# Performance work log

Hardware: AMD Instinct MI355X
Metric: run time of the kernel (lower is better)

## Reference

```python
import jax, jax.numpy as jnp
from jax import lax
import numpy as np

N_CLASS = 5
B, T = 2048, 2048


def setup_inputs() -> dict:
    key = jax.random.key(0)
    k1, k2 = jax.random.split(key)
    x = jax.random.normal(k1, (B, T, N_CLASS), dtype=jnp.float32)
    mask = jnp.ones((B, T), dtype=jnp.int32)
    transform = jax.random.normal(k2, (N_CLASS + 2, N_CLASS + 2), dtype=jnp.float32)
    return {"x": x, "mask": mask, "transform": transform}


def reference(x, mask, transform):
    # Batched Viterbi decode. x:[B,T,C], mask:[B,T], transform:[C+2,C+2]
    Bb, Tt, C = x.shape
    START, END = C, C + 1
    trans = transform[:C, :C]                      # [C,C] prev -> curr
    mb = mask.astype(bool)

    dp0 = x[:, 0, :] + transform[START, :C][None]  # [B,C]

    def step(dp, inp):
        xt, mt = inp                               # xt:[B,C], mt:[B]
        sc = dp[:, :, None] + trans[None]          # [B,C_prev,C_curr]
        bp = jnp.argmax(sc, axis=1)                # [B,C]
        new_dp = jnp.max(sc, axis=1) + xt          # [B,C]
        dp_out = jnp.where(mt[:, None], new_dp, dp)
        # identity backpointer on padded steps so backtrace is a no-op there
        bp_out = jnp.where(mt[:, None], bp, jnp.arange(C)[None, :])
        return dp_out, bp_out

    xs = (jnp.moveaxis(x[:, 1:, :], 1, 0),         # [T-1,B,C]
          jnp.moveaxis(mb[:, 1:], 1, 0))           # [T-1,B]
    dp, bps = lax.scan(step, dp0, xs)              # bps: [T-1,B,C]

    final = dp + transform[:C, END][None]          # [B,C]
    max_score = jnp.max(final, axis=1)             # [B]
    last = jnp.argmax(final, axis=1)               # [B]

    def back(idx, bp):
        prev = jnp.take_along_axis(bp, idx[:, None], axis=1)[:, 0]
        return prev, idx

    first, rest = lax.scan(back, last, bps, reverse=True)  # rest: [T-1,B]
    path = jnp.concatenate([first[None], rest], axis=0)    # [T,B]
    return max_score, path.T                                # [B], [B,T]
```

## Files before the change

### kernel.cpp

```cpp
#include <hip/hip_runtime.h>
#include <cstdint>

#define B_    2048
#define T_    2048
#define TD    7
#define NCHK  128
#define IDENT 0x4688u

__device__ __forceinline__ uint32_t mcompose(uint32_t f, uint32_t g) {
    uint32_t r = 0;
#pragma unroll
    for (int j = 0; j < 5; ++j) {
        uint32_t gj = (g >> (3 * j)) & 7u;
        r |= ((f >> (3 * gj)) & 7u) << (3 * j);
    }
    return r;
}

__device__ __forceinline__ uint32_t cvtpk(float lo, float hi) {
    uint32_t r;
    asm("v_cvt_pk_bf16_f32 %0, %1, %2" : "=v"(r) : "v"(lo), "v"(hi));
    return r;
}

__device__ __forceinline__ float bfld(const uint16_t* __restrict__ xs, int h) {
    return __uint_as_float(((uint32_t)xs[h]) << 16);
}

template<bool P>
__device__ __forceinline__ void hstep(const uint16_t* __restrict__ xs, int h, bool pred,
                                      float (&dp)[5], const float (&tr)[5][5]) {
    float nd[5];
#pragma unroll
    for (int j = 0; j < 5; ++j) {
        float v = fmaxf(fmaxf(fmaxf(fmaxf(dp[0] + tr[0][j], dp[1] + tr[1][j]),
                                    dp[2] + tr[2][j]), dp[3] + tr[3][j]),
                        dp[4] + tr[4][j]);
        nd[j] = v + bfld(xs, h + j);
    }
#pragma unroll
    for (int j = 0; j < 5; ++j) dp[j] = (P && !pred) ? dp[j] : nd[j];
}

template<bool SEL>
__device__ __forceinline__ uint32_t lstep(const uint16_t* __restrict__ xs, int h, bool mm,
                                          float (&dp)[5], const float (&tr)[5][5],
                                          uint32_t& rho) {
    float nd[5]; int aa[5]; uint32_t pk = 0;
#pragma unroll
    for (int j = 0; j < 5; ++j) {
        float s[5];
#pragma unroll
        for (int i = 0; i < 5; ++i) {
            float f = dp[i] + tr[i][j];
            uint32_t u = (__float_as_uint(f) & ~7u) | (uint32_t)(7 - i);
            s[i] = __uint_as_float(u);
        }
        float m = fmaxf(fmaxf(fmaxf(fmaxf(s[0], s[1]), s[2]), s[3]), s[4]);
        int a = 7 - (int)(__float_as_uint(m) & 7u);
        float v = m + bfld(xs, h + j);
        if (SEL) { a = mm ? a : j; nd[j] = mm ? v : dp[j]; }
        else     { nd[j] = v; }
        aa[j] = a;
        pk |= ((uint32_t)a) << (3 * j);
    }
    uint32_t nr = 0;
#pragma unroll
    for (int j = 0; j < 5; ++j) nr |= ((rho >> (3 * aa[j])) & 7u) << (3 * j);
    rho = nr;
#pragma unroll
    for (int j = 0; j < 5; ++j) dp[j] = nd[j];
    return pk;
}

template<bool AM>
__device__ __forceinline__ void fwd(const uint16_t* __restrict__ xs,
                                    const uint16_t* __restrict__ msk, int cc,
                                    const float (&tr)[5][5], const float (&ts)[5],
                                    float (&dp)[5], float (&dpE)[5],
                                    uint32_t (&acc)[8], uint32_t& rho) {
    const int hbase = (cc > 0) ? 82 * (cc - 1) : 0;
#pragma unroll
    for (int j = 0; j < 5; ++j) dp[j] = bfld(xs, hbase + j);
    if (cc <= 1) {
#pragma unroll
        for (int j = 0; j < 5; ++j) dp[j] += ts[j];
    }
    const uint32_t mh = AM ? 0xFFFFu : ((cc > 0) ? (uint32_t)msk[cc - 1] : 0u);
#pragma unroll
    for (int h = 1; h <= 15; ++h) {
        if (AM) hstep<false>(xs, hbase + 5 * h, true, dp, tr);
        else    hstep<true >(xs, hbase + 5 * h, ((mh >> h) & 1u) != 0, dp, tr);
    }
    if (AM && cc == 0) {
#pragma unroll
        for (int j = 0; j < 5; ++j) dp[j] = bfld(xs, j) + ts[j];
    }
#pragma unroll
    for (int j = 0; j < 5; ++j) dpE[j] = (cc == 0) ? 0.0f : dp[j];

    rho = IDENT;
    const int lb = 82 * cc;
    const uint32_t ml = AM ? 0xFFFFu : (uint32_t)msk[cc];
    acc[0] = lstep<true>(xs, lb, (cc != 0) && ((ml & 1u) != 0), dp, tr, rho);
#pragma unroll
    for (int l = 1; l < 16; ++l) {
        uint32_t pk;
        if (AM) pk = lstep<false>(xs, lb + 5 * l, true, dp, tr, rho);
        else    pk = lstep<true >(xs, lb + 5 * l, ((ml >> l) & 1u) != 0, dp, tr, rho);
        if (l & 1) acc[l >> 1] |= pk << 16;
        else       acc[l >> 1]  = pk;
    }
}

__global__ __launch_bounds__(128) void k_all(
    const float* __restrict__ x, const int* __restrict__ mask,
    const float* __restrict__ tf, float* __restrict__ out)
{
    __shared__ uint16_t xs[10496];
    __shared__ uint16_t msk[NCHK];
    __shared__ uint32_t tot[2];
    __shared__ float    part[2];
    __shared__ int      lastS;

    const int b = blockIdx.x, c = threadIdx.x;
    const int lane = c & 63, w = c >> 6;

    const float4* gx = (const float4*)(x + (size_t)b * (T_ * 5));
#pragma unroll
    for (int q = 0; q < 20; ++q) {
        int fi = c + 128 * q;
        float4 v = gx[fi];
        int e0 = 4 * fi;
        int k  = (e0 * 52429) >> 22;
        int h0 = e0 + 2 * k;
        *(uint32_t*)(xs + h0)     = cvtpk(v.x, v.y);
        *(uint32_t*)(xs + h0 + 2) = cvtpk(v.z, v.w);
    }
    uint32_t mb = 0;
    {
        const int4* gm = (const int4*)(mask + (size_t)b * T_);
#pragma unroll
        for (int q = 0; q < 4; ++q) {
            int4 a = gm[4 * c + q];
            mb |= (a.x ? 1u : 0u) << (4 * q);
            mb |= (a.y ? 1u : 0u) << (4 * q + 1);
            mb |= (a.z ? 1u : 0u) << (4 * q + 2);
            mb |= (a.w ? 1u : 0u) << (4 * q + 3);
        }
        msk[c] = (uint16_t)mb;
    }

    float tr[5][5], ts[5], te[5];
#pragma unroll
    for (int i = 0; i < 5; ++i)
#pragma unroll
        for (int j = 0; j < 5; ++j) tr[i][j] = tf[i * TD + j];
#pragma unroll
    for (int j = 0; j < 5; ++j) ts[j] = tf[5 * TD + j];
#pragma unroll
    for (int j = 0; j < 5; ++j) te[j] = tf[j * TD + 6];

    const int allones = __syncthreads_and(mb == 0xFFFFu);

    float dp[5], dpE[5]; uint32_t acc[8], rho;
    if (allones) fwd<true >(xs, msk, c, tr, ts, dp, dpE, acc, rho);
    else         fwd<false>(xs, msk, c, tr, ts, dp, dpE, acc, rho);

    float svec[5];
#pragma unroll
    for (int j = 0; j < 5; ++j) {
        int r = (rho >> (3 * j)) & 7;
        float e = dpE[0];
        e = (r == 1) ? dpE[1] : e;
        e = (r == 2) ? dpE[2] : e;
        e = (r == 3) ? dpE[3] : e;
        e = (r == 4) ? dpE[4] : e;
        svec[j] = dp[j] - e;
    }

    uint32_t I = rho;
#pragma unroll
    for (int d = 1; d < 64; d <<= 1) {
        uint32_t oth = __shfl_down(I, d);
        uint32_t cm  = mcompose(I, oth);
        I = (lane + d < 64) ? cm : I;
    }
    if (lane == 0) tot[w] = I;
    if (c == NCHK - 1) {
        float best = dp[0] + te[0]; int last = 0;
#pragma unroll
        for (int j = 1; j < 5; ++j) {
            float s = dp[j] + te[j];
            if (s > best) { best = s; last = j; }
        }
        lastS = last;
    }
    __syncthreads();

    uint32_t Tw = (w == 0) ? tot[1] : IDENT;
    uint32_t Ex = __shfl_down(I, 1);
    uint32_t M  = (lane < 63) ? mcompose(Ex, Tw) : Tw;
    const int last = lastS;
    const int ec = (M >> (3 * last)) & 7;

    {
        float v = svec[0];
        v = (ec == 1) ? svec[1] : v;
        v = (ec == 2) ? svec[2] : v;
        v = (ec == 3) ? svec[3] : v;
        v = (ec == 4) ? svec[4] : v;
        if (c == NCHK - 1) v += te[last];
#pragma unroll
        for (int off = 1; off < 64; off <<= 1) v += __shfl_xor(v, off);
        if (lane == 0) part[w] = v;
    }
    __syncthreads();
    if (c == 0) out[b] = part[0] + part[1];

    float pv[16];
    int e = ec;
#pragma unroll
    for (int l = 15; l >= 0; --l) {
        pv[l] = (float)e;
        uint32_t p = (acc[l >> 1] >> (16 * (l & 1))) & 0xFFFFu;
        e = (p >> (3 * e)) & 7;
    }
    float* path = out + B_ + (size_t)b * T_ + c * 16;
#pragma unroll
    for (int q = 0; q < 4; ++q) {
        float4 v; v.x = pv[4*q]; v.y = pv[4*q+1]; v.z = pv[4*q+2]; v.w = pv[4*q+3];
        ((float4*)path)[q] = v;
    }
}

extern "C" void kernel_launch(void* const* d_in, const int* in_sizes, int n_in,
                              void* d_out, int out_size, void* d_ws, size_t ws_size,
                              hipStream_t stream) {
    const float* x         = (const float*)d_in[0];
    const int*   mask      = (const int*)d_in[1];
    const float* transform = (const float*)d_in[2];
    float*       out       = (float*)d_out;

    hipLaunchKernelGGL(k_all, dim3(B_), dim3(128), 0, stream,
                       x, mask, transform, out);
}
```

Before: 40.68 us.

## Process two rows per block, prefetching the second row into registers during the first

Each block now handles two batch rows. The second row's x and mask are loaded into registers before the first row is computed, and a sched_barrier keeps those loads from sinking, so global-load latency overlaps the first row's forward pass. The shared buffer is refilled after a barrier. This halves the grid, sets launch bounds to a minimum of 2 blocks, and holds about 80 extra VGPRs for the prefetched data, which may lower occupancy.

```diff
diff --git a/kernel.cpp b/kernel.cpp
--- a/kernel.cpp
+++ b/kernel.cpp
@@ -26,6 +26,7 @@
 __device__ __forceinline__ float bfld(const uint16_t* __restrict__ xs, int h) {
     return __uint_as_float(((uint32_t)xs[h]) << 16);
 }
+
 
 template<bool P>
 __device__ __forceinline__ void hstep(const uint16_t* __restrict__ xs, int h, bool pred,
@@ -113,7 +114,125 @@
     }
 }
 
-__global__ __launch_bounds__(128) void k_all(
+template<bool AM>
+__device__ __forceinline__ void compute_row(
+    const uint16_t* __restrict__ xs, const uint16_t* __restrict__ msk,
+    uint32_t* __restrict__ tot, float* __restrict__ part, int* __restrict__ lastS,
+    int c, int lane, int w, int row,
+    const float (&tr)[5][5], const float (&ts)[5], const float (&te)[5],
+    float* __restrict__ out)
+{
+    float dp[5], dpE[5]; uint32_t acc[8], rho;
+    fwd<AM>(xs, msk, c, tr, ts, dp, dpE, acc, rho);
+
+    float svec[5];
+#pragma unroll
+    for (int j = 0; j < 5; ++j) {
+        int r = (rho >> (3 * j)) & 7;
+        float e = dpE[0];
+        e = (r == 1) ? dpE[1] : e;
+        e = (r == 2) ? dpE[2] : e;
+        e = (r == 3) ? dpE[3] : e;
+        e = (r == 4) ? dpE[4] : e;
+        svec[j] = dp[j] - e;
+    }
+
+    uint32_t I = rho;
+#pragma unroll
+    for (int d = 1; d < 64; d <<= 1) {
+        uint32_t oth = __shfl_down(I, d);
+        uint32_t cm  = mcompose(I, oth);
+        I = (lane + d < 64) ? cm : I;
+    }
+    if (lane == 0) tot[w] = I;
+    if (c == NCHK - 1) {
+        float best = dp[0] + te[0]; int last = 0;
+#pragma unroll
+        for (int j = 1; j < 5; ++j) {
+            float s = dp[j] + te[j];
+            if (s > best) { best = s; last = j; }
+        }
+        *lastS = last;
+    }
+    __syncthreads();
+
+    uint32_t Tw = (w == 0) ? tot[1] : IDENT;
+    uint32_t Ex = __shfl_down(I, 1);
+    uint32_t M  = (lane < 63) ? mcompose(Ex, Tw) : Tw;
+    const int last = *lastS;
+    const int ec = (M >> (3 * last)) & 7;
+
+    {
+        float v = svec[0];
+        v = (ec == 1) ? svec[1] : v;
+        v = (ec == 2) ? svec[2] : v;
+        v = (ec == 3) ? svec[3] : v;
+        v = (ec == 4) ? svec[4] : v;
+        if (c == NCHK - 1) v += te[last];
+#pragma unroll
+        for (int off = 1; off < 64; off <<= 1) v += __shfl_xor(v, off);
+        if (lane == 0) part[w] = v;
+    }
+    __syncthreads();
+    if (c == 0) out[row] = part[0] + part[1];
+
+    float pv[16];
+    int e = ec;
+#pragma unroll
+    for (int l = 15; l >= 0; --l) {
+        pv[l] = (float)e;
+        uint32_t p = (acc[l >> 1] >> (16 * (l & 1))) & 0xFFFFu;
+        e = (p >> (3 * e)) & 7;
+    }
+    float* path = out + B_ + (size_t)row * T_ + c * 16;
+#pragma unroll
+    for (int q = 0; q < 4; ++q) {
+        float4 v; v.x = pv[4*q]; v.y = pv[4*q+1]; v.z = pv[4*q+2]; v.w = pv[4*q+3];
+        ((float4*)path)[q] = v;
+    }
+}
+
+
+struct XR { float4 v[10]; };
+struct MR { int4 m[4]; };
+
+__device__ __forceinline__ void load_row(const float4* __restrict__ gx,
+                                         const int4* __restrict__ gm, int c,
+                                         XR& a, XR& b, MR& mr) {
+#pragma unroll
+    for (int q = 0; q < 10; ++q) a.v[q] = gx[c + 128 * q];
+#pragma unroll
+    for (int q = 0; q < 10; ++q) b.v[q] = gx[c + 128 * (10 + q)];
+#pragma unroll
+    for (int q = 0; q < 4; ++q) mr.m[q] = gm[4 * c + q];
+}
+
+__device__ __forceinline__ void write_half(uint16_t* __restrict__ xs, int c, int off,
+                                           const XR& r) {
+#pragma unroll
+    for (int q = 0; q < 10; ++q) {
+        int fi = c + 128 * (off + q);
+        int e0 = 4 * fi;
+        int k  = (e0 * 52429) >> 22;
+        int h0 = e0 + 2 * k;
+        *(uint32_t*)(xs + h0)     = cvtpk(r.v[q].x, r.v[q].y);
+        *(uint32_t*)(xs + h0 + 2) = cvtpk(r.v[q].z, r.v[q].w);
+    }
+}
+
+__device__ __forceinline__ uint32_t mask_bits(const MR& mr) {
+    uint32_t mb = 0;
+#pragma unroll
+    for (int q = 0; q < 4; ++q) {
+        mb |= (mr.m[q].x ? 1u : 0u) << (4 * q);
+        mb |= (mr.m[q].y ? 1u : 0u) << (4 * q + 1);
+        mb |= (mr.m[q].z ? 1u : 0u) << (4 * q + 2);
+        mb |= (mr.m[q].w ? 1u : 0u) << (4 * q + 3);
+    }
+    return mb;
+}
+
+__global__ __launch_bounds__(128, 2) void k_all(
     const float* __restrict__ x, const int* __restrict__ mask,
     const float* __restrict__ tf, float* __restrict__ out)
 {
@@ -123,33 +242,14 @@
     __shared__ float    part[2];
     __shared__ int      lastS;
 
-    const int b = blockIdx.x, c = threadIdx.x;
+    const int c = threadIdx.x;
     const int lane = c & 63, w = c >> 6;
-
-    const float4* gx = (const float4*)(x + (size_t)b * (T_ * 5));
-#pragma unroll
-    for (int q = 0; q < 20; ++q) {
-        int fi = c + 128 * q;
-        float4 v = gx[fi];
-        int e0 = 4 * fi;
-        int k  = (e0 * 52429) >> 22;
-        int h0 = e0 + 2 * k;
-        *(uint32_t*)(xs + h0)     = cvtpk(v.x, v.y);
-        *(uint32_t*)(xs + h0 + 2) = cvtpk(v.z, v.w);
-    }
-    uint32_t mb = 0;
-    {
-        const int4* gm = (const int4*)(mask + (size_t)b * T_);
-#pragma unroll
-        for (int q = 0; q < 4; ++q) {
-            int4 a = gm[4 * c + q];
-            mb |= (a.x ? 1u : 0u) << (4 * q);
-            mb |= (a.y ? 1u : 0u) << (4 * q + 1);
-            mb |= (a.z ? 1u : 0u) << (4 * q + 2);
-            mb |= (a.w ? 1u : 0u) << (4 * q + 3);
-        }
-        msk[c] = (uint16_t)mb;
-    }
+    const int row0 = 2 * blockIdx.x, row1 = row0 + 1;
+
+    const float4* gx0 = (const float4*)(x + (size_t)row0 * (T_ * 5));
+    const int4*   gm0 = (const int4*)(mask + (size_t)row0 * T_);
+    const float4* gx1 = (const float4*)(x + (size_t)row1 * (T_ * 5));
+    const int4*   gm1 = (const int4*)(mask + (size_t)row1 * T_);
 
     float tr[5][5], ts[5], te[5];
 #pragma unroll
@@ -161,77 +261,31 @@
 #pragma unroll
     for (int j = 0; j < 5; ++j) te[j] = tf[j * TD + 6];
 
-    const int allones = __syncthreads_and(mb == 0xFFFFu);
-
-    float dp[5], dpE[5]; uint32_t acc[8], rho;
-    if (allones) fwd<true >(xs, msk, c, tr, ts, dp, dpE, acc, rho);
-    else         fwd<false>(xs, msk, c, tr, ts, dp, dpE, acc, rho);
-
-    float svec[5];
-#pragma unroll
-    for (int j = 0; j < 5; ++j) {
-        int r = (rho >> (3 * j)) & 7;
-        float e = dpE[0];
-        e = (r == 1) ? dpE[1] : e;
-        e = (r == 2) ? dpE[2] : e;
-        e = (r == 3) ? dpE[3] : e;
-        e = (r == 4) ? dpE[4] : e;
-        svec[j] = dp[j] - e;
-    }
-
-    uint32_t I = rho;
-#pragma unroll
-    for (int d = 1; d < 64; d <<= 1) {
-        uint32_t oth = __shfl_down(I, d);
-        uint32_t cm  = mcompose(I, oth);
-        I = (lane + d < 64) ? cm : I;
-    }
-    if (lane == 0) tot[w] = I;
-    if (c == NCHK - 1) {
-        float best = dp[0] + te[0]; int last = 0;
-#pragma unroll
-        for (int j = 1; j < 5; ++j) {
-            float s = dp[j] + te[j];
-            if (s > best) { best = s; last = j; }
-        }
-        lastS = last;
-    }
+    XR a0, b0; MR mr0;
+    load_row(gx0, gm0, c, a0, b0, mr0);
+    write_half(xs, c, 0, a0);
+    write_half(xs, c, 10, b0);
+    uint32_t mb0 = mask_bits(mr0);
+    msk[c] = (uint16_t)mb0;
+    const int am0 = __syncthreads_and(mb0 == 0xFFFFu);
+
+    XR a1, b1; MR mr1;
+    load_row(gx1, gm1, c, a1, b1, mr1);
+    __builtin_amdgcn_sched_barrier(0);
+
+    if (am0) compute_row<true >(xs, msk, tot, part, &lastS, c, lane, w, row0, tr, ts, te, out);
+    else     compute_row<false>(xs, msk, tot, part, &lastS, c, lane, w, row0, tr, ts, te, out);
+
     __syncthreads();
 
-    uint32_t Tw = (w == 0) ? tot[1] : IDENT;
-    uint32_t Ex = __shfl_down(I, 1);
-    uint32_t M  = (lane < 63) ? mcompose(Ex, Tw) : Tw;
-    const int last = lastS;
-    const int ec = (M >> (3 * last)) & 7;
-
-    {
-        float v = svec[0];
-        v = (ec == 1) ? svec[1] : v;
-        v = (ec == 2) ? svec[2] : v;
-        v = (ec == 3) ? svec[3] : v;
-        v = (ec == 4) ? svec[4] : v;
-        if (c == NCHK - 1) v += te[last];
-#pragma unroll
-        for (int off = 1; off < 64; off <<= 1) v += __shfl_xor(v, off);
-        if (lane == 0) part[w] = v;
-    }
-    __syncthreads();
-    if (c == 0) out[b] = part[0] + part[1];
-
-    float pv[16];
-    int e = ec;
-#pragma unroll
-    for (int l = 15; l >= 0; --l) {
-        pv[l] = (float)e;
-        uint32_t p = (acc[l >> 1] >> (16 * (l & 1))) & 0xFFFFu;
-        e = (p >> (3 * e)) & 7;
-    }
-    float* path = out + B_ + (size_t)b * T_ + c * 16;
-#pragma unroll
-    for (int q = 0; q < 4; ++q) {
-        float4 v; v.x = pv[4*q]; v.y = pv[4*q+1]; v.z = pv[4*q+2]; v.w = pv[4*q+3];
-        ((float4*)path)[q] = v;
-    }
+    write_half(xs, c, 0, a1);
+    write_half(xs, c, 10, b1);
+    uint32_t mb1 = mask_bits(mr1);
+    msk[c] = (uint16_t)mb1;
+    const int am1 = __syncthreads_and(mb1 == 0xFFFFu);
+
+    if (am1) compute_row<true >(xs, msk, tot, part, &lastS, c, lane, w, row1, tr, ts, te, out);
+    else     compute_row<false>(xs, msk, tot, part, &lastS, c, lane, w, row1, tr, ts, te, out);
 }
 
 extern "C" void kernel_launch(void* const* d_in, const int* in_sizes, int n_in,
@@ -242,6 +296,6 @@
     const float* transform = (const float*)d_in[2];
     float*       out       = (float*)d_out;
 
-    hipLaunchKernelGGL(k_all, dim3(B_), dim3(128), 0, stream,
+    hipLaunchKernelGGL(k_all, dim3(B_ / 2), dim3(128), 0, stream,
                        x, mask, transform, out);
 }
```

Result: no change. 40.23 us (-1.1%).

## Use one wavefront per sequence with 32-step chunks and swizzled LDS vector loads

Applied to the files above, without the earlier changes.

The block shrinks from 128 to 64 threads, so each lane handles a 32-step chunk and the cross-wave shared-memory combine and barriers go away. Emission data is stored in LDS with a rotating swizzle and read as uint4 vectors into registers, replacing per-element 16-bit LDS loads. The mask is packed with wave ballots instead of per-thread int4 loads. The trade-off is half as many threads per sequence, so the serial chain per lane is longer, plus higher register pressure from the word buffers.

```diff
diff --git a/kernel.cpp b/kernel.cpp
--- a/kernel.cpp
+++ b/kernel.cpp
@@ -4,7 +4,6 @@
 #define B_    2048
 #define T_    2048
 #define TD    7
-#define NCHK  128
 #define IDENT 0x4688u
 
 __device__ __forceinline__ uint32_t mcompose(uint32_t f, uint32_t g) {
@@ -23,12 +22,19 @@
     return r;
 }
 
-__device__ __forceinline__ float bfld(const uint16_t* __restrict__ xs, int h) {
-    return __uint_as_float(((uint32_t)xs[h]) << 16);
+__device__ __forceinline__ float xget(const uint32_t* w, int h) {
+    return (h & 1) ? __uint_as_float(w[h >> 1] & 0xFFFF0000u)
+                   : __uint_as_float(w[h >> 1] << 16);
+}
+
+__device__ __forceinline__ int gidx(int cc, int q) {
+    int s = q + (cc & 7);
+    s = (s >= 20) ? s - 20 : s;
+    return 20 * cc + s;
 }
 
 template<bool P>
-__device__ __forceinline__ void hstep(const uint16_t* __restrict__ xs, int h, bool pred,
+__device__ __forceinline__ void hstep(const uint32_t* w, int base, bool pred,
                                       float (&dp)[5], const float (&tr)[5][5]) {
     float nd[5];
 #pragma unroll
@@ -36,14 +42,14 @@
         float v = fmaxf(fmaxf(fmaxf(fmaxf(dp[0] + tr[0][j], dp[1] + tr[1][j]),
                                     dp[2] + tr[2][j]), dp[3] + tr[3][j]),
                         dp[4] + tr[4][j]);
-        nd[j] = v + bfld(xs, h + j);
+        nd[j] = v + xget(w, base + j);
     }
 #pragma unroll
     for (int j = 0; j < 5; ++j) dp[j] = (P && !pred) ? dp[j] : nd[j];
 }
 
 template<bool SEL>
-__device__ __forceinline__ uint32_t lstep(const uint16_t* __restrict__ xs, int h, bool mm,
+__device__ __forceinline__ uint32_t lstep(const uint32_t* w, int base, bool mm,
                                           float (&dp)[5], const float (&tr)[5][5],
                                           uint32_t& rho) {
     float nd[5]; int aa[5]; uint32_t pk = 0;
@@ -58,7 +64,7 @@
         }
         float m = fmaxf(fmaxf(fmaxf(fmaxf(s[0], s[1]), s[2]), s[3]), s[4]);
         int a = 7 - (int)(__float_as_uint(m) & 7u);
-        float v = m + bfld(xs, h + j);
+        float v = m + xget(w, base + j);
         if (SEL) { a = mm ? a : j; nd[j] = mm ? v : dp[j]; }
         else     { nd[j] = v; }
         aa[j] = a;
@@ -73,82 +79,41 @@
     return pk;
 }
 
-template<bool AM>
-__device__ __forceinline__ void fwd(const uint16_t* __restrict__ xs,
-                                    const uint16_t* __restrict__ msk, int cc,
-                                    const float (&tr)[5][5], const float (&ts)[5],
-                                    float (&dp)[5], float (&dpE)[5],
-                                    uint32_t (&acc)[8], uint32_t& rho) {
-    const int hbase = (cc > 0) ? 82 * (cc - 1) : 0;
-#pragma unroll
-    for (int j = 0; j < 5; ++j) dp[j] = bfld(xs, hbase + j);
-    if (cc <= 1) {
-#pragma unroll
-        for (int j = 0; j < 5; ++j) dp[j] += ts[j];
-    }
-    const uint32_t mh = AM ? 0xFFFFu : ((cc > 0) ? (uint32_t)msk[cc - 1] : 0u);
-#pragma unroll
-    for (int h = 1; h <= 15; ++h) {
-        if (AM) hstep<false>(xs, hbase + 5 * h, true, dp, tr);
-        else    hstep<true >(xs, hbase + 5 * h, ((mh >> h) & 1u) != 0, dp, tr);
-    }
-    if (AM && cc == 0) {
-#pragma unroll
-        for (int j = 0; j < 5; ++j) dp[j] = bfld(xs, j) + ts[j];
-    }
-#pragma unroll
-    for (int j = 0; j < 5; ++j) dpE[j] = (cc == 0) ? 0.0f : dp[j];
-
-    rho = IDENT;
-    const int lb = 82 * cc;
-    const uint32_t ml = AM ? 0xFFFFu : (uint32_t)msk[cc];
-    acc[0] = lstep<true>(xs, lb, (cc != 0) && ((ml & 1u) != 0), dp, tr, rho);
-#pragma unroll
-    for (int l = 1; l < 16; ++l) {
-        uint32_t pk;
-        if (AM) pk = lstep<false>(xs, lb + 5 * l, true, dp, tr, rho);
-        else    pk = lstep<true >(xs, lb + 5 * l, ((ml >> l) & 1u) != 0, dp, tr, rho);
-        if (l & 1) acc[l >> 1] |= pk << 16;
-        else       acc[l >> 1]  = pk;
-    }
-}
-
-__global__ __launch_bounds__(128) void k_all(
+__global__ __launch_bounds__(64) void k_all(
     const float* __restrict__ x, const int* __restrict__ mask,
     const float* __restrict__ tf, float* __restrict__ out)
 {
-    __shared__ uint16_t xs[10496];
-    __shared__ uint16_t msk[NCHK];
-    __shared__ uint32_t tot[2];
-    __shared__ float    part[2];
-    __shared__ int      lastS;
-
+    __shared__ __align__(16) uint16_t xs[10240];
     const int b = blockIdx.x, c = threadIdx.x;
-    const int lane = c & 63, w = c >> 6;
 
     const float4* gx = (const float4*)(x + (size_t)b * (T_ * 5));
-#pragma unroll
-    for (int q = 0; q < 20; ++q) {
-        int fi = c + 128 * q;
+    const int*    gi = mask + (size_t)b * T_;
+
+#pragma unroll
+    for (int qi = 0; qi < 40; ++qi) {
+        int fi = c + 64 * qi;
         float4 v = gx[fi];
-        int e0 = 4 * fi;
-        int k  = (e0 * 52429) >> 22;
-        int h0 = e0 + 2 * k;
-        *(uint32_t*)(xs + h0)     = cvtpk(v.x, v.y);
-        *(uint32_t*)(xs + h0 + 2) = cvtpk(v.z, v.w);
-    }
+        uint32_t e0 = 4u * (uint32_t)fi;
+        uint32_t co = e0 / 160u;
+        uint32_t el = e0 - 160u * co;
+        uint32_t q  = el >> 3;
+        uint32_t s  = q + (co & 7u); s = (s >= 20u) ? s - 20u : s;
+        uint32_t ha = 160u * co + 8u * s + (el & 7u);
+        uint2 p; p.x = cvtpk(v.x, v.y); p.y = cvtpk(v.z, v.w);
+        *(uint2*)(xs + ha) = p;
+    }
+
     uint32_t mb = 0;
     {
-        const int4* gm = (const int4*)(mask + (size_t)b * T_);
-#pragma unroll
-        for (int q = 0; q < 4; ++q) {
-            int4 a = gm[4 * c + q];
-            mb |= (a.x ? 1u : 0u) << (4 * q);
-            mb |= (a.y ? 1u : 0u) << (4 * q + 1);
-            mb |= (a.z ? 1u : 0u) << (4 * q + 2);
-            mb |= (a.w ? 1u : 0u) << (4 * q + 3);
-        }
-        msk[c] = (uint16_t)mb;
+        int mv[32];
+#pragma unroll
+        for (int q = 0; q < 32; ++q) mv[q] = gi[c + 64 * q];
+#pragma unroll
+        for (int q = 0; q < 32; ++q) {
+            unsigned long long bal = __ballot(mv[q] != 0);
+            if (c == 2 * q)     mb = (uint32_t)bal;
+            if (c == 2 * q + 1) mb = (uint32_t)(bal >> 32);
+        }
     }
 
     float tr[5][5], ts[5], te[5];
@@ -161,11 +126,76 @@
 #pragma unroll
     for (int j = 0; j < 5; ++j) te[j] = tf[j * TD + 6];
 
-    const int allones = __syncthreads_and(mb == 0xFFFFu);
-
-    float dp[5], dpE[5]; uint32_t acc[8], rho;
-    if (allones) fwd<true >(xs, msk, c, tr, ts, dp, dpE, acc, rho);
-    else         fwd<false>(xs, msk, c, tr, ts, dp, dpE, acc, rho);
+    const bool allm = __all(mb == 0xFFFFFFFFu);
+    uint32_t mh = __shfl_up(mb, 1);
+    mh = (c > 0) ? (mh >> 16) : 0u;
+
+    __syncthreads();
+
+    const uint4* xsv = (const uint4*)xs;
+    const int hc = (c > 0) ? c - 1 : 0;
+
+    uint32_t hwA[20], hwB[20];
+#pragma unroll
+    for (int k = 0; k < 5; ++k) {
+        uint4 t = xsv[gidx(hc, 10 + k)];
+        hwA[4*k] = t.x; hwA[4*k+1] = t.y; hwA[4*k+2] = t.z; hwA[4*k+3] = t.w;
+    }
+#pragma unroll
+    for (int k = 0; k < 5; ++k) {
+        uint4 t = xsv[gidx(hc, 15 + k)];
+        hwB[4*k] = t.x; hwB[4*k+1] = t.y; hwB[4*k+2] = t.z; hwB[4*k+3] = t.w;
+    }
+    float dp[5];
+#pragma unroll
+    for (int j = 0; j < 5; ++j) dp[j] = xget(hwA, j);
+    if (allm) {
+#pragma unroll
+        for (int h = 1; h <= 7; ++h)  hstep<false>(hwA, 5 * h, true, dp, tr);
+#pragma unroll
+        for (int h = 8; h <= 15; ++h) hstep<false>(hwB, 5 * (h - 8), true, dp, tr);
+    } else {
+#pragma unroll
+        for (int h = 1; h <= 7; ++h)  hstep<true>(hwA, 5 * h, ((mh >> h) & 1u) != 0, dp, tr);
+#pragma unroll
+        for (int h = 8; h <= 15; ++h) hstep<true>(hwB, 5 * (h - 8), ((mh >> h) & 1u) != 0, dp, tr);
+    }
+    if (c == 0) {
+        uint4 t0 = xsv[gidx(0, 0)];
+        uint32_t w0[4] = { t0.x, t0.y, t0.z, t0.w };
+#pragma unroll
+        for (int j = 0; j < 5; ++j) dp[j] = xget(w0, j) + ts[j];
+    }
+    float dpE[5];
+#pragma unroll
+    for (int j = 0; j < 5; ++j) dpE[j] = (c == 0) ? 0.0f : dp[j];
+
+    uint32_t acc[16];
+    uint32_t rho = IDENT;
+#pragma unroll
+    for (int bb = 0; bb < 4; ++bb) {
+        uint32_t w[20];
+#pragma unroll
+        for (int k = 0; k < 5; ++k) {
+            uint4 t = xsv[gidx(c, 5 * bb + k)];
+            w[4*k] = t.x; w[4*k+1] = t.y; w[4*k+2] = t.z; w[4*k+3] = t.w;
+        }
+#pragma unroll
+        for (int ll = 0; ll < 8; ++ll) {
+            const int l = 8 * bb + ll;
+            uint32_t pk;
+            if (l == 0) {
+                bool mm = (c != 0) && ((mb & 1u) != 0);
+                pk = lstep<true>(w, 0, mm, dp, tr, rho);
+            } else if (allm) {
+                pk = lstep<false>(w, 5 * ll, true, dp, tr, rho);
+            } else {
+                pk = lstep<true>(w, 5 * ll, ((mb >> l) & 1u) != 0, dp, tr, rho);
+            }
+            if (l & 1) acc[l >> 1] |= pk << 16;
+            else       acc[l >> 1]  = pk;
+        }
+    }
 
     float svec[5];
 #pragma unroll
@@ -184,24 +214,17 @@
     for (int d = 1; d < 64; d <<= 1) {
         uint32_t oth = __shfl_down(I, d);
         uint32_t cm  = mcompose(I, oth);
-        I = (lane + d < 64) ? cm : I;
-    }
-    if (lane == 0) tot[w] = I;
-    if (c == NCHK - 1) {
-        float best = dp[0] + te[0]; int last = 0;
-#pragma unroll
-        for (int j = 1; j < 5; ++j) {
-            float s = dp[j] + te[j];
-            if (s > best) { best = s; last = j; }
-        }
-        lastS = last;
-    }
-    __syncthreads();
-
-    uint32_t Tw = (w == 0) ? tot[1] : IDENT;
-    uint32_t Ex = __shfl_down(I, 1);
-    uint32_t M  = (lane < 63) ? mcompose(Ex, Tw) : Tw;
-    const int last = lastS;
+        I = (c + d < 64) ? cm : I;
+    }
+    float best = dp[0] + te[0]; int lastv = 0;
+#pragma unroll
+    for (int j = 1; j < 5; ++j) {
+        float s = dp[j] + te[j];
+        if (s > best) { best = s; lastv = j; }
+    }
+    const int last = __shfl(lastv, 63);
+    uint32_t M = __shfl_down(I, 1);
+    M = (c < 63) ? M : IDENT;
     const int ec = (M >> (3 * last)) & 7;
 
     {
@@ -210,25 +233,23 @@
         v = (ec == 2) ? svec[2] : v;
         v = (ec == 3) ? svec[3] : v;
         v = (ec == 4) ? svec[4] : v;
-        if (c == NCHK - 1) v += te[last];
+        if (c == 63) v += te[last];
 #pragma unroll
         for (int off = 1; off < 64; off <<= 1) v += __shfl_xor(v, off);
-        if (lane == 0) part[w] = v;
-    }
-    __syncthreads();
-    if (c == 0) out[b] = part[0] + part[1];
-
-    float pv[16];
+        if (c == 0) out[b] = v;
+    }
+
+    float pv[32];
     int e = ec;
 #pragma unroll
-    for (int l = 15; l >= 0; --l) {
+    for (int l = 31; l >= 0; --l) {
         pv[l] = (float)e;
         uint32_t p = (acc[l >> 1] >> (16 * (l & 1))) & 0xFFFFu;
         e = (p >> (3 * e)) & 7;
     }
-    float* path = out + B_ + (size_t)b * T_ + c * 16;
-#pragma unroll
-    for (int q = 0; q < 4; ++q) {
+    float* path = out + B_ + (size_t)b * T_ + c * 32;
+#pragma unroll
+    for (int q = 0; q < 8; ++q) {
         float4 v; v.x = pv[4*q]; v.y = pv[4*q+1]; v.z = pv[4*q+2]; v.w = pv[4*q+3];
         ((float4*)path)[q] = v;
     }
@@ -242,6 +263,6 @@
     const float* transform = (const float*)d_in[2];
     float*       out       = (float*)d_out;
 
-    hipLaunchKernelGGL(k_all, dim3(B_), dim3(128), 0, stream,
+    hipLaunchKernelGGL(k_all, dim3(B_), dim3(64), 0, stream,
                        x, mask, transform, out);
 }
```

Result: faster. 37.69 us (-7.3%).
